# Kernel optimization log

Hardware: AMD Instinct MI355X
Metric: run time of the kernel (lower is better)

Reference implementation:

```python
import jax, jax.numpy as jnp
import numpy as np

N_HEAD = 16
D_HEAD = 64
D_MODEL = 1024
LN_EPS = 1e-5


def layer_norm(x, gamma, beta):
    mu = jnp.mean(x, axis=-1, keepdims=True)
    var = jnp.mean((x - mu) ** 2, axis=-1, keepdims=True)
    return (x - mu) * jax.lax.rsqrt(var + LN_EPS) * gamma + beta


def setup_inputs() -> dict:
    key = jax.random.key(0)
    ks = jax.random.split(key, 6)
    B, T = 2, 2048
    inp = jax.random.normal(ks[0], (B, T, D_MODEL), dtype=jnp.float32)
    # qkv_net: Linear(d_model, 3*n_head*d_head)
    W_qkv = jax.random.normal(ks[1], (3 * N_HEAD * D_HEAD, D_MODEL), dtype=jnp.float32) * (D_MODEL ** -0.5)
    b_qkv = jax.random.normal(ks[2], (3 * N_HEAD * D_HEAD,), dtype=jnp.float32) * 0.02
    # o_net: Linear(n_head*d_head, d_model, bias=False)
    W_o = jax.random.normal(ks[3], (D_MODEL, N_HEAD * D_HEAD), dtype=jnp.float32) * ((N_HEAD * D_HEAD) ** -0.5)
    gamma = jnp.ones((D_MODEL,), dtype=jnp.float32)
    beta = jnp.zeros((D_MODEL,), dtype=jnp.float32)
    return {"inp": inp, "W_qkv": W_qkv, "b_qkv": b_qkv, "W_o": W_o, "gamma": gamma, "beta": beta}


def reference(inp, W_qkv, b_qkv, W_o, gamma, beta):
    B, T, D = inp.shape
    H, dh = N_HEAD, D_HEAD
    scale = 1.0 / (dh ** 0.5)

    qkv = inp @ W_qkv.T + b_qkv                      # (B, T, 3*H*dh)
    head_q, head_k, head_v = jnp.split(qkv, 3, axis=2)
    # (B, T, H, dh) -> (B, H, T, dh)
    q = head_q.reshape(B, T, H, dh).transpose(0, 2, 1, 3)
    k = head_k.reshape(B, T, H, dh).transpose(0, 2, 1, 3)
    v = head_v.reshape(B, T, H, dh).transpose(0, 2, 1, 3)

    attn_score = jnp.einsum('bhqd,bhkd->bhqk', q, k) * scale  # (B, H, T, T)
    attn_prob = jax.nn.softmax(attn_score, axis=-1)           # dropatt is identity in eval
    attn_vec = jnp.einsum('bhqk,bhkd->bhqd', attn_prob, v)    # (B, H, T, dh)

    # Faithful to original: (B*H, T, dh) batch-major buffer is VIEWED as (H, B, T, dh)
    attn_vec = attn_vec.reshape(H, B, T, dh)
    attn_vec = attn_vec.transpose(1, 2, 0, 3).reshape(B, T, H * dh)

    attn_out = attn_vec @ W_o.T                                # dropout identity in eval
    return layer_norm(inp + attn_out, gamma, beta)
```

## Files before the change

### kernel.cpp

```cpp
#include <hip/hip_runtime.h>
#include <hip/hip_bf16.h>
#include <stdint.h>

typedef __bf16 bf16_t;
typedef __bf16 bf16x8 __attribute__((ext_vector_type(8)));
typedef __bf16 bf16x4 __attribute__((ext_vector_type(4)));
typedef __bf16 bf16x2 __attribute__((ext_vector_type(2)));
typedef float floatx4 __attribute__((ext_vector_type(4)));

#define QSCALE 0.180336879f

#if __has_builtin(__builtin_amdgcn_cvt_pk_bf16_f32)
#define HAS_PK_BF16 1
#endif

__device__ static inline void gll16(const void* g, void* l) {
    __builtin_amdgcn_global_load_lds((const __attribute__((address_space(1))) void*)g,
                                     (__attribute__((address_space(3))) void*)l, 16, 0, 0);
}

__device__ static inline bf16x8 pack8(const float* p) {
    bf16x8 o;
#ifdef HAS_PK_BF16
#pragma unroll
    for (int j = 0; j < 4; j++) {
        bf16x2 t2 = __builtin_amdgcn_cvt_pk_bf16_f32(p[2 * j], p[2 * j + 1]);
        o[2 * j] = t2[0]; o[2 * j + 1] = t2[1];
    }
#else
#pragma unroll
    for (int j = 0; j < 8; j++) o[j] = (bf16_t)p[j];
#endif
    return o;
}

__global__ __launch_bounds__(256) void cvt_all(const float* __restrict__ inp,
                                               const float* __restrict__ wqkv,
                                               const float* __restrict__ wo,
                                               bf16_t* __restrict__ o_inp,
                                               bf16_t* __restrict__ o_wqkv,
                                               bf16_t* __restrict__ o_wo) {
    int blk = blockIdx.x;
    const float* src;
    bf16_t* dst;
    if (blk < 4096)      { src = inp;  dst = o_inp; }
    else if (blk < 7168) { src = wqkv; dst = o_wqkv; blk -= 4096; }
    else                 { src = wo;   dst = o_wo;   blk -= 7168; }
    int i = blk * 256 + threadIdx.x;
    float4 v = ((const float4*)src)[i];
    float p[4] = {v.x, v.y, v.z, v.w};
    bf16x4 o;
#ifdef HAS_PK_BF16
    bf16x2 t0 = __builtin_amdgcn_cvt_pk_bf16_f32(p[0], p[1]);
    bf16x2 t1 = __builtin_amdgcn_cvt_pk_bf16_f32(p[2], p[3]);
    o[0] = t0[0]; o[1] = t0[1]; o[2] = t1[0]; o[3] = t1[1];
#else
    o[0] = (bf16_t)p[0]; o[1] = (bf16_t)p[1]; o[2] = (bf16_t)p[2]; o[3] = (bf16_t)p[3];
#endif
    ((bf16x4*)dst)[i] = o;
}

__global__ __launch_bounds__(256, 3)
void gemm_qkv(const bf16_t* __restrict__ A, const bf16_t* __restrict__ Bw,
              const float* __restrict__ bias,
              bf16_t* __restrict__ qk, bf16_t* __restrict__ vT) {
    constexpr int K = 1024;
    __shared__ bf16_t lA[3][128 * 32];
    __shared__ bf16_t lB[3][128 * 32];
    const int tid  = threadIdx.x;
    const int lane = tid & 63, wave = tid >> 6;
    const int quad = lane >> 4, l16 = lane & 15;
    const int wy = wave >> 1, wx = wave & 1;

    const int L  = blockIdx.y * 24 + blockIdx.x;
    const int nL = (L & 7) * 96 + (L >> 3);
    const int bm = (nL / 24) * 128, bn = (nL % 24) * 128;

    const int c0 = tid, c1 = tid + 256;
    const int k0 = ((c0 & 3) ^ ((c0 >> 3) & 3)) * 8;
    const int k1 = ((c1 & 3) ^ ((c1 >> 3) & 3)) * 8;
    const bf16_t* Ap0 = A + (size_t)(bm + (c0 >> 2)) * K + k0;
    const bf16_t* Ap1 = A + (size_t)(bm + (c1 >> 2)) * K + k1;
    const bf16_t* Bp0 = Bw + (size_t)(bn + (c0 >> 2)) * K + k0;
    const bf16_t* Bp1 = Bw + (size_t)(bn + (c1 >> 2)) * K + k1;
    const int d0 = (wave * 64) * 8;
    const int d1 = (256 + wave * 64) * 8;

    const int sq8 = (quad ^ ((l16 >> 1) & 3)) * 8;

    floatx4 acc[4][4] = {};

    gll16(Ap0, &lA[0][d0]); gll16(Ap1, &lA[0][d1]);
    gll16(Bp0, &lB[0][d0]); gll16(Bp1, &lB[0][d1]);
    gll16(Ap0 + 32, &lA[1][d0]); gll16(Ap1 + 32, &lA[1][d1]);
    gll16(Bp0 + 32, &lB[1][d0]); gll16(Bp1 + 32, &lB[1][d1]);

    int cur = 0;
    for (int it = 0; it < 32; ++it) {
        if (it < 31) {
            asm volatile("s_waitcnt vmcnt(4)" ::: "memory");
        } else {
            asm volatile("s_waitcnt vmcnt(0)" ::: "memory");
        }
        __builtin_amdgcn_s_barrier();
        if (it < 30) {
            const int kt = (it + 2) * 32;
            const int nb = cur >= 1 ? cur - 1 : 2;
            gll16(Ap0 + kt, &lA[nb][d0]); gll16(Ap1 + kt, &lA[nb][d1]);
            gll16(Bp0 + kt, &lB[nb][d0]); gll16(Bp1 + kt, &lB[nb][d1]);
        }
        __builtin_amdgcn_sched_barrier(0);

        bf16x8 af[4], bfr[4];
#pragma unroll
        for (int i = 0; i < 4; i++) {
            af[i]  = *(const bf16x8*)(&lA[cur][(wy * 64 + i * 16 + l16) * 32 + sq8]);
            bfr[i] = *(const bf16x8*)(&lB[cur][(wx * 64 + i * 16 + l16) * 32 + sq8]);
        }
#pragma unroll
        for (int i = 0; i < 4; i++)
#pragma unroll
            for (int j = 0; j < 4; j++)
                acc[i][j] = __builtin_amdgcn_mfma_f32_16x16x32_bf16(af[i], bfr[j], acc[i][j], 0, 0, 0);

        cur = cur < 2 ? cur + 1 : 0;
    }

    const bool is_v = (bn >= 2048);
#pragma unroll
    for (int j = 0; j < 4; j++) {
        const int n = bn + wx * 64 + j * 16 + l16;
        const float bv = bias[n];
        const bool isq = (n < 1024);
#pragma unroll
        for (int i = 0; i < 4; i++) {
            const int mbase = bm + wy * 64 + i * 16 + quad * 4;
            if (!is_v) {
#pragma unroll
                for (int r = 0; r < 4; r++) {
                    float c = acc[i][j][r] + bv;
                    if (isq) c *= QSCALE;
                    qk[(size_t)(mbase + r) * 2048 + n] = (bf16_t)c;
                }
            } else {
                const int nn = n - 2048;
                const int b  = mbase >> 11;
                const int t  = mbase & 2047;
                const int vrow = b * 1024 + nn;
                const int pcol = (t & ~31) | (((t >> 2) & 3) << 3) | (((t >> 4) & 1) << 2);
                bf16x4 pack;
#pragma unroll
                for (int r = 0; r < 4; r++) pack[r] = (bf16_t)(acc[i][j][r] + bv);
                *(bf16x4*)(vT + (size_t)vrow * 2048 + pcol) = pack;
            }
        }
    }
}

__global__ __launch_bounds__(512, 4)
void attn_kernel(const bf16_t* __restrict__ qk, const bf16_t* __restrict__ vT,
                 bf16_t* __restrict__ Ofin) {
    __shared__ bf16_t Kbuf[3][64 * 64];
    __shared__ bf16_t Vbuf[3][64 * 64];
    const int tid  = threadIdx.x;
    const int lane = tid & 63, wave = tid >> 6;
    const int quad = lane >> 4, l16 = lane & 15;
    const int bid = blockIdx.x;
    const int s    = bid & 31;
    const int hl   = ((s & 7) << 2) | ((s >> 3) & 3);
    const int qt   = bid >> 5;
    const int b = hl >> 4, h = hl & 15;

    const bf16_t* Qbase = qk + (size_t)(b * 2048 + qt * 128 + wave * 16) * 2048 + h * 64;
    const bf16_t* Kbase = qk + (size_t)(b * 2048) * 2048 + 1024 + h * 64;
    const bf16_t* Vbase = vT + (size_t)(hl * 64) * 2048;

    const int srow  = (tid >> 2) & 63;
    const int dhalf = tid >> 8;
    const int sc8 = ((tid & 3) ^ ((tid >> 3) & 3)) * 8;
    const bf16_t* Kg = Kbase + (size_t)srow * 2048 + dhalf * 32 + sc8;
    const bf16_t* Vg = Vbase + (size_t)srow * 2048 + dhalf * 32 + sc8;
    const int wbase = wave * 512;

    const int xq8 = (quad ^ ((l16 >> 1) & 3)) * 8;

    floatx4 accO[4] = {};
    floatx4 accL = {};
    bf16x8 onesf;
#pragma unroll
    for (int j = 0; j < 8; j++) onesf[j] = (bf16_t)1.0f;

    bf16x8 qf[2];
#pragma unroll
    for (int kc = 0; kc < 2; kc++)
        qf[kc] = *(const bf16x8*)(Qbase + (size_t)l16 * 2048 + kc * 32 + quad * 8);

    gll16(Kg, &Kbuf[0][wbase]);
    gll16(Vg, &Vbuf[0][wbase]);
    gll16(Kg + (size_t)64 * 2048, &Kbuf[1][wbase]);
    gll16(Vg + 64, &Vbuf[1][wbase]);

    int cur = 0;
    for (int it = 0; it < 32; ++it) {
        if (it < 31) {
            asm volatile("s_waitcnt vmcnt(2)" ::: "memory");
        } else {
            asm volatile("s_waitcnt vmcnt(0)" ::: "memory");
        }
        __builtin_amdgcn_s_barrier();
        if (it < 30) {
            const int nb = cur >= 1 ? cur - 1 : 2;
            gll16(Kg + (size_t)(it + 2) * 64 * 2048, &Kbuf[nb][wbase]);
            gll16(Vg + (it + 2) * 64, &Vbuf[nb][wbase]);
        }
        __builtin_amdgcn_sched_barrier(0);

        floatx4 st[4] = {};
        __builtin_amdgcn_s_setprio(1);
#pragma unroll
        for (int nt = 0; nt < 4; nt++) {
            bf16x8 k0 = *(const bf16x8*)&Kbuf[cur][(nt * 16 + l16) * 32 + xq8];
            bf16x8 k1 = *(const bf16x8*)&Kbuf[cur][2048 + (nt * 16 + l16) * 32 + xq8];
            st[nt] = __builtin_amdgcn_mfma_f32_16x16x32_bf16(k0, qf[0], st[nt], 0, 0, 0);
            st[nt] = __builtin_amdgcn_mfma_f32_16x16x32_bf16(k1, qf[1], st[nt], 0, 0, 0);
        }
        __builtin_amdgcn_s_setprio(0);

        bf16x8 vf[2][4];
#pragma unroll
        for (int kc2 = 0; kc2 < 2; kc2++)
#pragma unroll
            for (int ct = 0; ct < 4; ct++)
                vf[kc2][ct] = *(const bf16x8*)&Vbuf[cur][kc2 * 2048 + (ct * 16 + l16) * 32 + xq8];
        bf16x8 pf[2];
#pragma unroll
        for (int kc2 = 0; kc2 < 2; kc2++) {
            float p[8];
#pragma unroll
            for (int j = 0; j < 8; j++)
                p[j] = __builtin_amdgcn_exp2f(st[kc2 * 2 + (j >> 2)][j & 3]);
            pf[kc2] = pack8(p);
        }
        __builtin_amdgcn_s_setprio(1);
#pragma unroll
        for (int kc2 = 0; kc2 < 2; kc2++) {
#pragma unroll
            for (int ct = 0; ct < 4; ct++)
                accO[ct] = __builtin_amdgcn_mfma_f32_16x16x32_bf16(pf[kc2], vf[kc2][ct], accO[ct], 0, 0, 0);
            accL = __builtin_amdgcn_mfma_f32_16x16x32_bf16(pf[kc2], onesf, accL, 0, 0, 0);
        }
        __builtin_amdgcn_s_setprio(0);

        cur = cur < 2 ? cur + 1 : 0;
    }

    float linv[4];
#pragma unroll
    for (int r = 0; r < 4; r++) linv[r] = 1.0f / accL[r];

    const int b2 = hl & 1;
    const int colb = hl >> 1;
    const int rowb = b2 * 2048 + qt * 128 + wave * 16;
    bf16_t* outb = Ofin + (size_t)rowb * 1024 + colb * 64;
#pragma unroll
    for (int ct = 0; ct < 4; ct++)
#pragma unroll
        for (int r = 0; r < 4; r++)
            outb[(size_t)(quad * 4 + r) * 1024 + ct * 16 + l16] =
                (bf16_t)(accO[ct][r] * linv[r]);
}

__global__ __launch_bounds__(256, 4)
void gemm_o(const bf16_t* __restrict__ Op, const bf16_t* __restrict__ Bw,
            bf16_t* __restrict__ out) {
    constexpr int K = 1024;
    __shared__ bf16_t lA[3][64 * 32];
    __shared__ bf16_t lB[3][128 * 32];
    const int tid  = threadIdx.x;
    const int lane = tid & 63, wave = tid >> 6;
    const int quad = lane >> 4, l16 = lane & 15;
    const int wy = wave >> 1, wx = wave & 1;

    const int L  = blockIdx.y * 8 + blockIdx.x;
    const int nL = (L & 7) * 64 + (L >> 3);
    const int bm = (nL >> 3) * 64, bn = (nL & 7) * 128;

    const int akc = ((tid & 3) ^ ((tid >> 3) & 3)) * 8;
    const bf16_t* Ap = Op + (size_t)(bm + (tid >> 2)) * K + akc;
    const int dA = wave * 512;
    const int cb0 = tid, cb1 = tid + 256;
    const int bk0 = ((cb0 & 3) ^ ((cb0 >> 3) & 3)) * 8;
    const int bk1 = ((cb1 & 3) ^ ((cb1 >> 3) & 3)) * 8;
    const bf16_t* Bp0 = Bw + (size_t)(bn + (cb0 >> 2)) * K + bk0;
    const bf16_t* Bp1 = Bw + (size_t)(bn + (cb1 >> 2)) * K + bk1;
    const int d0 = wave * 512;
    const int d1 = 2048 + wave * 512;

    const int xq8 = (quad ^ ((l16 >> 1) & 3)) * 8;

    gll16(Ap, &lA[0][dA]);
    gll16(Bp0, &lB[0][d0]); gll16(Bp1, &lB[0][d1]);
    gll16(Ap + 32, &lA[1][dA]);
    gll16(Bp0 + 32, &lB[1][d0]); gll16(Bp1 + 32, &lB[1][d1]);

    floatx4 acc[2][4] = {};
    int cur = 0;
    for (int it = 0; it < 32; ++it) {
        if (it < 31) {
            asm volatile("s_waitcnt vmcnt(3)" ::: "memory");
        } else {
            asm volatile("s_waitcnt vmcnt(0)" ::: "memory");
        }
        __builtin_amdgcn_s_barrier();
        if (it < 30) {
            const int kt = (it + 2) * 32;
            const int nb = cur >= 1 ? cur - 1 : 2;
            gll16(Ap + kt, &lA[nb][dA]);
            gll16(Bp0 + kt, &lB[nb][d0]); gll16(Bp1 + kt, &lB[nb][d1]);
        }
        __builtin_amdgcn_sched_barrier(0);

        bf16x8 af[2], bfr[4];
#pragma unroll
        for (int i = 0; i < 2; i++)
            af[i] = *(const bf16x8*)(&lA[cur][(wy * 32 + i * 16 + l16) * 32 + xq8]);
#pragma unroll
        for (int j = 0; j < 4; j++)
            bfr[j] = *(const bf16x8*)(&lB[cur][(wx * 64 + j * 16 + l16) * 32 + xq8]);
#pragma unroll
        for (int i = 0; i < 2; i++)
#pragma unroll
            for (int j = 0; j < 4; j++)
                acc[i][j] = __builtin_amdgcn_mfma_f32_16x16x32_bf16(af[i], bfr[j], acc[i][j], 0, 0, 0);

        cur = cur < 2 ? cur + 1 : 0;
    }
#pragma unroll
    for (int j = 0; j < 4; j++) {
        const int n = bn + wx * 64 + j * 16 + l16;
#pragma unroll
        for (int i = 0; i < 2; i++) {
            const int mbase = bm + wy * 32 + i * 16 + quad * 4;
#pragma unroll
            for (int r = 0; r < 4; r++)
                out[(size_t)(mbase + r) * 1024 + n] = (bf16_t)acc[i][j][r];
        }
    }
}

__global__ __launch_bounds__(256)
void ln_kernel(const float* __restrict__ inp, const bf16_t* __restrict__ ao,
               const float* __restrict__ gamma, const float* __restrict__ beta,
               float* __restrict__ out) {
    const int row = blockIdx.x, tid = threadIdx.x;
    const int wave = tid >> 6, lane = tid & 63;
    float4 a = ((const float4*)(inp + (size_t)row * 1024))[tid];
    bf16x4 c4 = ((const bf16x4*)(ao + (size_t)row * 1024))[tid];
    float x0 = a.x + (float)c4[0], x1 = a.y + (float)c4[1];
    float x2 = a.z + (float)c4[2], x3 = a.w + (float)c4[3];
    float s = x0 + x1 + x2 + x3;
    float sq = x0 * x0 + x1 * x1 + x2 * x2 + x3 * x3;
#pragma unroll
    for (int mm = 32; mm >= 1; mm >>= 1) {
        s += __shfl_xor(s, mm);
        sq += __shfl_xor(sq, mm);
    }
    __shared__ float rs[4], rq[4];
    if (lane == 0) { rs[wave] = s; rq[wave] = sq; }
    __syncthreads();
    s = rs[0] + rs[1] + rs[2] + rs[3];
    sq = rq[0] + rq[1] + rq[2] + rq[3];
    const float mu = s * (1.0f / 1024.0f);
    const float var = sq * (1.0f / 1024.0f) - mu * mu;
    const float rstd = rsqrtf(var + 1e-5f);
    float4 g = ((const float4*)gamma)[tid], bt = ((const float4*)beta)[tid];
    float4 o;
    o.x = (x0 - mu) * rstd * g.x + bt.x;
    o.y = (x1 - mu) * rstd * g.y + bt.y;
    o.z = (x2 - mu) * rstd * g.z + bt.z;
    o.w = (x3 - mu) * rstd * g.w + bt.w;
    ((float4*)(out + (size_t)row * 1024))[tid] = o;
}

extern "C" void kernel_launch(void* const* d_in, const int* in_sizes, int n_in,
                              void* d_out, int out_size, void* d_ws, size_t ws_size,
                              hipStream_t stream) {
    const float* inp   = (const float*)d_in[0];
    const float* Wqkv  = (const float*)d_in[1];
    const float* bqkv  = (const float*)d_in[2];
    const float* Wo    = (const float*)d_in[3];
    const float* gamma = (const float*)d_in[4];
    const float* beta  = (const float*)d_in[5];
    float* out = (float*)d_out;

    char* ws = (char*)d_ws;
    bf16_t* inp_bf  = (bf16_t*)(ws);
    bf16_t* wqkv_bf = (bf16_t*)(ws + (8u << 20));
    bf16_t* wo_bf   = (bf16_t*)(ws + (14u << 20));
    bf16_t* qk_buf  = (bf16_t*)(ws + (16u << 20));
    bf16_t* vT_buf  = (bf16_t*)(ws + (32u << 20));
    bf16_t* ao_bf   = (bf16_t*)(ws + (32u << 20));
    bf16_t* ofin    = (bf16_t*)(ws + (48u << 20));

    cvt_all<<<8192, 256, 0, stream>>>(inp, Wqkv, Wo, inp_bf, wqkv_bf, wo_bf);
    gemm_qkv<<<dim3(24, 32), 256, 0, stream>>>(inp_bf, wqkv_bf, bqkv, qk_buf, vT_buf);
    attn_kernel<<<512, 512, 0, stream>>>(qk_buf, vT_buf, ofin);
    gemm_o<<<dim3(8, 64), 256, 0, stream>>>(ofin, wo_bf, ao_bf);
    ln_kernel<<<4096, 256, 0, stream>>>(inp, ao_bf, gamma, beta, out);
}
```

Measured before the change: 188.4 us.

## Software-pipeline attention loop: overlap next QK^T with previous PV using 4-stage buffers

Restructures the attention inner loop so iteration it computes S for tile it while doing exp and the P·V MMA for tile it-1, with a drain step after the loop. LDS ring grows from 3 to 4 slots so the V tile for the previous iteration stays valid while new loads land. Launch bounds drop to 2 blocks per CU to allow more registers for the held-over scores, and the setprio hints are removed. The aim is to hide exp/pack latency behind independent MFMA work, at the cost of higher register and LDS use and lower occupancy.

```diff
diff --git a/kernel.cpp b/kernel.cpp
--- a/kernel.cpp
+++ b/kernel.cpp
@@ -157,11 +157,11 @@
     }
 }
 
-__global__ __launch_bounds__(512, 4)
+__global__ __launch_bounds__(512, 2)
 void attn_kernel(const bf16_t* __restrict__ qk, const bf16_t* __restrict__ vT,
                  bf16_t* __restrict__ Ofin) {
-    __shared__ bf16_t Kbuf[3][64 * 64];
-    __shared__ bf16_t Vbuf[3][64 * 64];
+    __shared__ bf16_t Kbuf[4][64 * 64];
+    __shared__ bf16_t Vbuf[4][64 * 64];
     const int tid  = threadIdx.x;
     const int lane = tid & 63, wave = tid >> 6;
     const int quad = lane >> 4, l16 = lane & 15;
@@ -200,7 +200,7 @@
     gll16(Kg + (size_t)64 * 2048, &Kbuf[1][wbase]);
     gll16(Vg + 64, &Vbuf[1][wbase]);
 
-    int cur = 0;
+    floatx4 st_prev[4];
     for (int it = 0; it < 32; ++it) {
         if (it < 31) {
             asm volatile("s_waitcnt vmcnt(2)" ::: "memory");
@@ -209,39 +209,66 @@
         }
         __builtin_amdgcn_s_barrier();
         if (it < 30) {
-            const int nb = cur >= 1 ? cur - 1 : 2;
+            const int nb = (it + 2) & 3;
             gll16(Kg + (size_t)(it + 2) * 64 * 2048, &Kbuf[nb][wbase]);
             gll16(Vg + (it + 2) * 64, &Vbuf[nb][wbase]);
         }
         __builtin_amdgcn_sched_barrier(0);
 
+        const int kb = it & 3;
         floatx4 st[4] = {};
-        __builtin_amdgcn_s_setprio(1);
 #pragma unroll
         for (int nt = 0; nt < 4; nt++) {
-            bf16x8 k0 = *(const bf16x8*)&Kbuf[cur][(nt * 16 + l16) * 32 + xq8];
-            bf16x8 k1 = *(const bf16x8*)&Kbuf[cur][2048 + (nt * 16 + l16) * 32 + xq8];
+            bf16x8 k0 = *(const bf16x8*)&Kbuf[kb][(nt * 16 + l16) * 32 + xq8];
+            bf16x8 k1 = *(const bf16x8*)&Kbuf[kb][2048 + (nt * 16 + l16) * 32 + xq8];
             st[nt] = __builtin_amdgcn_mfma_f32_16x16x32_bf16(k0, qf[0], st[nt], 0, 0, 0);
             st[nt] = __builtin_amdgcn_mfma_f32_16x16x32_bf16(k1, qf[1], st[nt], 0, 0, 0);
         }
-        __builtin_amdgcn_s_setprio(0);
-
+        if (it > 0) {
+            const int vb = (it - 1) & 3;
+            bf16x8 vf[2][4];
+#pragma unroll
+            for (int kc2 = 0; kc2 < 2; kc2++)
+#pragma unroll
+                for (int ct = 0; ct < 4; ct++)
+                    vf[kc2][ct] = *(const bf16x8*)&Vbuf[vb][kc2 * 2048 + (ct * 16 + l16) * 32 + xq8];
+            bf16x8 pf[2];
+#pragma unroll
+            for (int kc2 = 0; kc2 < 2; kc2++) {
+                float p[8];
+#pragma unroll
+                for (int j = 0; j < 8; j++)
+                    p[j] = __builtin_amdgcn_exp2f(st_prev[kc2 * 2 + (j >> 2)][j & 3]);
+                pf[kc2] = pack8(p);
+            }
+#pragma unroll
+            for (int kc2 = 0; kc2 < 2; kc2++) {
+#pragma unroll
+                for (int ct = 0; ct < 4; ct++)
+                    accO[ct] = __builtin_amdgcn_mfma_f32_16x16x32_bf16(pf[kc2], vf[kc2][ct], accO[ct], 0, 0, 0);
+                accL = __builtin_amdgcn_mfma_f32_16x16x32_bf16(pf[kc2], onesf, accL, 0, 0, 0);
+            }
+        }
+#pragma unroll
+        for (int nt = 0; nt < 4; nt++) st_prev[nt] = st[nt];
+    }
+    {
+        const int vb = 31 & 3;
         bf16x8 vf[2][4];
 #pragma unroll
         for (int kc2 = 0; kc2 < 2; kc2++)
 #pragma unroll
             for (int ct = 0; ct < 4; ct++)
-                vf[kc2][ct] = *(const bf16x8*)&Vbuf[cur][kc2 * 2048 + (ct * 16 + l16) * 32 + xq8];
+                vf[kc2][ct] = *(const bf16x8*)&Vbuf[vb][kc2 * 2048 + (ct * 16 + l16) * 32 + xq8];
         bf16x8 pf[2];
 #pragma unroll
         for (int kc2 = 0; kc2 < 2; kc2++) {
             float p[8];
 #pragma unroll
             for (int j = 0; j < 8; j++)
-                p[j] = __builtin_amdgcn_exp2f(st[kc2 * 2 + (j >> 2)][j & 3]);
+                p[j] = __builtin_amdgcn_exp2f(st_prev[kc2 * 2 + (j >> 2)][j & 3]);
             pf[kc2] = pack8(p);
         }
-        __builtin_amdgcn_s_setprio(1);
 #pragma unroll
         for (int kc2 = 0; kc2 < 2; kc2++) {
 #pragma unroll
@@ -249,9 +276,6 @@
                 accO[ct] = __builtin_amdgcn_mfma_f32_16x16x32_bf16(pf[kc2], vf[kc2][ct], accO[ct], 0, 0, 0);
             accL = __builtin_amdgcn_mfma_f32_16x16x32_bf16(pf[kc2], onesf, accL, 0, 0, 0);
         }
-        __builtin_amdgcn_s_setprio(0);
-
-        cur = cur < 2 ? cur + 1 : 0;
     }
 
     float linv[4];
```

Result: faster. 182.8 us (-3.0%).

## Process two K/V tiles per barrier with four-slot LDS ring

Applied to the files above, without the earlier changes.

Restructures the attention main loop to handle two 64-key tiles per iteration. It uses a 4-deep K/V LDS ring and prefetches the next two tiles right after one __syncthreads, replacing the per-tile explicit vmcnt wait and barrier. This halves the number of barriers and lets each wave do twice the MFMA work between synchronisations. In exchange, LDS per block grows to 64 KB and launch bounds drop to 2, which may cut resident blocks per CU. The full-drain barrier also waits on all outstanding loads each iteration.

```diff
diff --git a/kernel.cpp b/kernel.cpp
--- a/kernel.cpp
+++ b/kernel.cpp
@@ -157,11 +157,11 @@
     }
 }
 
-__global__ __launch_bounds__(512, 4)
+__global__ __launch_bounds__(512, 2)
 void attn_kernel(const bf16_t* __restrict__ qk, const bf16_t* __restrict__ vT,
                  bf16_t* __restrict__ Ofin) {
-    __shared__ bf16_t Kbuf[3][64 * 64];
-    __shared__ bf16_t Vbuf[3][64 * 64];
+    __shared__ bf16_t Kbuf[4][64 * 64];
+    __shared__ bf16_t Vbuf[4][64 * 64];
     const int tid  = threadIdx.x;
     const int lane = tid & 63, wave = tid >> 6;
     const int quad = lane >> 4, l16 = lane & 15;
@@ -200,58 +200,53 @@
     gll16(Kg + (size_t)64 * 2048, &Kbuf[1][wbase]);
     gll16(Vg + 64, &Vbuf[1][wbase]);
 
-    int cur = 0;
-    for (int it = 0; it < 32; ++it) {
-        if (it < 31) {
-            asm volatile("s_waitcnt vmcnt(2)" ::: "memory");
-        } else {
-            asm volatile("s_waitcnt vmcnt(0)" ::: "memory");
-        }
-        __builtin_amdgcn_s_barrier();
-        if (it < 30) {
-            const int nb = cur >= 1 ? cur - 1 : 2;
-            gll16(Kg + (size_t)(it + 2) * 64 * 2048, &Kbuf[nb][wbase]);
-            gll16(Vg + (it + 2) * 64, &Vbuf[nb][wbase]);
-        }
-        __builtin_amdgcn_sched_barrier(0);
-
-        floatx4 st[4] = {};
-        __builtin_amdgcn_s_setprio(1);
-#pragma unroll
-        for (int nt = 0; nt < 4; nt++) {
-            bf16x8 k0 = *(const bf16x8*)&Kbuf[cur][(nt * 16 + l16) * 32 + xq8];
-            bf16x8 k1 = *(const bf16x8*)&Kbuf[cur][2048 + (nt * 16 + l16) * 32 + xq8];
-            st[nt] = __builtin_amdgcn_mfma_f32_16x16x32_bf16(k0, qf[0], st[nt], 0, 0, 0);
-            st[nt] = __builtin_amdgcn_mfma_f32_16x16x32_bf16(k1, qf[1], st[nt], 0, 0, 0);
-        }
-        __builtin_amdgcn_s_setprio(0);
-
-        bf16x8 vf[2][4];
-#pragma unroll
-        for (int kc2 = 0; kc2 < 2; kc2++)
-#pragma unroll
-            for (int ct = 0; ct < 4; ct++)
-                vf[kc2][ct] = *(const bf16x8*)&Vbuf[cur][kc2 * 2048 + (ct * 16 + l16) * 32 + xq8];
-        bf16x8 pf[2];
-#pragma unroll
-        for (int kc2 = 0; kc2 < 2; kc2++) {
-            float p[8];
-#pragma unroll
-            for (int j = 0; j < 8; j++)
-                p[j] = __builtin_amdgcn_exp2f(st[kc2 * 2 + (j >> 2)][j & 3]);
-            pf[kc2] = pack8(p);
-        }
-        __builtin_amdgcn_s_setprio(1);
-#pragma unroll
-        for (int kc2 = 0; kc2 < 2; kc2++) {
-#pragma unroll
-            for (int ct = 0; ct < 4; ct++)
-                accO[ct] = __builtin_amdgcn_mfma_f32_16x16x32_bf16(pf[kc2], vf[kc2][ct], accO[ct], 0, 0, 0);
-            accL = __builtin_amdgcn_mfma_f32_16x16x32_bf16(pf[kc2], onesf, accL, 0, 0, 0);
-        }
-        __builtin_amdgcn_s_setprio(0);
-
-        cur = cur < 2 ? cur + 1 : 0;
+    for (int i = 0; i < 16; ++i) {
+        __syncthreads();
+        if (i < 15) {
+            const int t2 = 2 * i + 2, t3 = 2 * i + 3;
+            gll16(Kg + (size_t)t2 * 64 * 2048, &Kbuf[t2 & 3][wbase]);
+            gll16(Vg + t2 * 64,                &Vbuf[t2 & 3][wbase]);
+            gll16(Kg + (size_t)t3 * 64 * 2048, &Kbuf[t3 & 3][wbase]);
+            gll16(Vg + t3 * 64,                &Vbuf[t3 & 3][wbase]);
+        }
+#pragma unroll
+        for (int u = 0; u < 2; ++u) {
+            const int kb = (2 * i + u) & 3;
+            floatx4 st[4] = {};
+            __builtin_amdgcn_s_setprio(1);
+#pragma unroll
+            for (int nt = 0; nt < 4; nt++) {
+                bf16x8 k0 = *(const bf16x8*)&Kbuf[kb][(nt * 16 + l16) * 32 + xq8];
+                bf16x8 k1 = *(const bf16x8*)&Kbuf[kb][2048 + (nt * 16 + l16) * 32 + xq8];
+                st[nt] = __builtin_amdgcn_mfma_f32_16x16x32_bf16(k0, qf[0], st[nt], 0, 0, 0);
+                st[nt] = __builtin_amdgcn_mfma_f32_16x16x32_bf16(k1, qf[1], st[nt], 0, 0, 0);
+            }
+            __builtin_amdgcn_s_setprio(0);
+            bf16x8 vf[2][4];
+#pragma unroll
+            for (int kc2 = 0; kc2 < 2; kc2++)
+#pragma unroll
+                for (int ct = 0; ct < 4; ct++)
+                    vf[kc2][ct] = *(const bf16x8*)&Vbuf[kb][kc2 * 2048 + (ct * 16 + l16) * 32 + xq8];
+            bf16x8 pf[2];
+#pragma unroll
+            for (int kc2 = 0; kc2 < 2; kc2++) {
+                float p[8];
+#pragma unroll
+                for (int j = 0; j < 8; j++)
+                    p[j] = __builtin_amdgcn_exp2f(st[kc2 * 2 + (j >> 2)][j & 3]);
+                pf[kc2] = pack8(p);
+            }
+            __builtin_amdgcn_s_setprio(1);
+#pragma unroll
+            for (int kc2 = 0; kc2 < 2; kc2++) {
+#pragma unroll
+                for (int ct = 0; ct < 4; ct++)
+                    accO[ct] = __builtin_amdgcn_mfma_f32_16x16x32_bf16(pf[kc2], vf[kc2][ct], accO[ct], 0, 0, 0);
+                accL = __builtin_amdgcn_mfma_f32_16x16x32_bf16(pf[kc2], onesf, accL, 0, 0, 0);
+            }
+            __builtin_amdgcn_s_setprio(0);
+        }
     }
 
     float linv[4];
```

Result: no change. 191.8 us (+1.8%).
